# Optimization experiments

Hardware: AMD Instinct MI355X
Metric: run time of the kernel (lower is better)

## Reference

```python
import jax, jax.numpy as jnp
import numpy as np

BLOCK = 32
# MXFP4 grid: exp_bits=2, man_bits=1, exp_bias=1 -> {0, 0.5, 1, 1.5, 2, 3, 4, 6}
GRID = jnp.array([0.0, 0.5, 1.0, 1.5, 2.0, 3.0, 4.0, 6.0], dtype=jnp.float32)
GRID_MAX = 6.0
EPS = 1e-12


def _snap_to_grid(a):
    # nearest-neighbor snap; ties go to the lower grid value (matches torch ref)
    pos = jnp.searchsorted(GRID, a)              # side='left', same as torch default
    lo = jnp.clip(pos - 1, 0, GRID.shape[0] - 1)
    hi = jnp.clip(pos, 0, GRID.shape[0] - 1)
    v_lo = GRID[lo]
    v_hi = GRID[hi]
    return jnp.where(a - v_lo > v_hi - a, v_hi, v_lo)


def quant_act_mxfp4(x):
    orig_shape = x.shape
    xb = x.astype(jnp.float32).reshape(-1, BLOCK)           # [nblk, BLOCK]
    amax = jnp.clip(jnp.max(jnp.abs(xb), axis=-1, keepdims=True), EPS)
    # scale stored in FP16 (quant_act_fp hard-codes scale_dtype='FP16')
    scale = (amax / GRID_MAX).astype(jnp.float16).astype(jnp.float32)
    x_norm = xb / jnp.clip(scale, EPS)
    snapped = _snap_to_grid(jnp.abs(x_norm))
    return (jnp.sign(x_norm) * snapped * scale).reshape(orig_shape)


def setup_inputs() -> dict:
    key = jax.random.key(0)
    k1, k2, k3 = jax.random.split(key, 3)
    x = jax.random.normal(k1, (2, 4096, 4096), dtype=jnp.float32)
    W = jax.random.normal(k2, (11008, 4096), dtype=jnp.float32)
    bias = jax.random.normal(k3, (11008,), dtype=jnp.float32)
    return {"x": x, "W": W, "bias": bias}


def reference(x, W, bias):
    # 1) dynamic per-block MXFP4 activation quantization
    x_q = quant_act_mxfp4(x)                                # [B, S, H]
    # 2) dense GEMM: F.linear(x_q, W, bias)
    return jnp.einsum('bsh,oh->bso', x_q, W) + bias
```

## Files before the change

### kernel.cpp

```cpp
#include <hip/hip_runtime.h>


#define M_DIM 8192
#define K_DIM 4096
#define N_DIM 11008

typedef float floatx4 __attribute__((ext_vector_type(4)));
typedef _Float16 half8 __attribute__((ext_vector_type(8)));


__device__ inline float snap_mxfp4(float a) {
    float lo  = (a <= 0.25f) ? 0.0f : ((a <= 0.75f) ? 0.5f : 1.0f);
    float mid = (a <= 1.75f) ? 1.5f : 2.0f;
    float hi  = (a <= 3.5f)  ? 3.0f : ((a <= 5.0f) ? 4.0f : 6.0f);
    return (a <= 1.25f) ? lo : ((a <= 2.5f) ? mid : hi);
}

__global__ __launch_bounds__(256) void quant_x_kernel(
        const float* __restrict__ x, _Float16* __restrict__ xq) {
    size_t t    = (size_t)blockIdx.x * 256 + threadIdx.x;
    size_t base = t * 8;
    const float4* p = (const float4*)(x + base);
    float4 v0 = p[0];
    float4 v1 = p[1];
    float in[8] = {v0.x, v0.y, v0.z, v0.w, v1.x, v1.y, v1.z, v1.w};

    float a0 = fmaxf(fmaxf(fabsf(in[0]), fabsf(in[1])), fmaxf(fabsf(in[2]), fabsf(in[3])));
    float a1 = fmaxf(fmaxf(fabsf(in[4]), fabsf(in[5])), fmaxf(fabsf(in[6]), fabsf(in[7])));
    float amax = fmaxf(a0, a1);
    amax = fmaxf(amax, __shfl_xor(amax, 1));
    amax = fmaxf(amax, __shfl_xor(amax, 2));
    amax = fmaxf(amax, 1e-12f);

    float scale = (float)(_Float16)(amax / 6.0f);
    float sdiv  = fmaxf(scale, 1e-12f);

    union { _Float16 h[8]; uint4 v; } o;
#pragma unroll
    for (int i = 0; i < 8; ++i) {
        float xn = in[i] / sdiv;
        float s  = snap_mxfp4(fabsf(xn));
        o.h[i]   = (_Float16)copysignf(s * scale, xn);
    }
    *(uint4*)(xq + base) = o.v;
}


__global__ __launch_bounds__(256) void conv_w_kernel(
        const float* __restrict__ W, _Float16* __restrict__ Wq) {
    size_t t    = (size_t)blockIdx.x * 256 + threadIdx.x;
    size_t base = t * 8;
    const float4* p = (const float4*)(W + base);
    float4 v0 = p[0];
    float4 v1 = p[1];
    float in[8] = {v0.x, v0.y, v0.z, v0.w, v1.x, v1.y, v1.z, v1.w};
    union { _Float16 h[8]; uint4 v; } o;
#pragma unroll
    for (int i = 0; i < 8; ++i) o.h[i] = (_Float16)in[i];
    *(uint4*)(Wq + base) = o.v;
}


#define BM 128
#define BN 128
#define BK 32

__global__ __launch_bounds__(256) void gemm_f16_kernel(
        const _Float16* __restrict__ A, const _Float16* __restrict__ B,
        const float* __restrict__ bias, float* __restrict__ C) {
    __shared__ __align__(16) _Float16 sA[BM * BK];
    __shared__ __align__(16) _Float16 sB[BN * BK];

    const int tid   = threadIdx.x;
    const int lane  = tid & 63;
    const int wave  = tid >> 6;
    const int wr    = wave >> 1;
    const int wc    = wave & 1;
    const int mlane = lane & 15;
    const int kq    = lane >> 4;

    const int rowStart = blockIdx.y * BM;
    const int colStart = blockIdx.x * BN;

    const int p0 = tid, p1 = tid + 256;
    const int r0 = p0 >> 2, r1 = p1 >> 2;
    const int kc0 = (p0 & 3) ^ (r0 & 3);
    const int kc1 = (p1 & 3) ^ (r1 & 3);
    const _Float16* aSrc0 = A + (size_t)(rowStart + r0) * K_DIM + kc0 * 8;
    const _Float16* aSrc1 = A + (size_t)(rowStart + r1) * K_DIM + kc1 * 8;
    const _Float16* bSrc0 = B + (size_t)(colStart + r0) * K_DIM + kc0 * 8;
    const _Float16* bSrc1 = B + (size_t)(colStart + r1) * K_DIM + kc1 * 8;

    _Float16* ldsA0 = sA + (wave * 64) * 8;
    _Float16* ldsA1 = sA + (256 + wave * 64) * 8;
    _Float16* ldsB0 = sB + (wave * 64) * 8;
    _Float16* ldsB1 = sB + (256 + wave * 64) * 8;

    int aOff[4], bOff[4];
#pragma unroll
    for (int i = 0; i < 4; ++i) {
        int row = wr * 64 + i * 16 + mlane;
        aOff[i] = (row * 4 + (kq ^ (row & 3))) * 8;
        int col = wc * 64 + i * 16 + mlane;
        bOff[i] = (col * 4 + (kq ^ (col & 3))) * 8;
    }

    floatx4 acc[4][4];
    const floatx4 z4 = {0.f, 0.f, 0.f, 0.f};
#pragma unroll
    for (int i = 0; i < 4; ++i)
#pragma unroll
        for (int j = 0; j < 4; ++j) acc[i][j] = z4;

    for (int k0 = 0; k0 < K_DIM; k0 += BK) {
        __builtin_amdgcn_global_load_lds(
            (const __attribute__((address_space(1))) unsigned int*)(const void*)(aSrc0 + k0),
            (__attribute__((address_space(3))) unsigned int*)(void*)ldsA0, 16, 0, 0);
        __builtin_amdgcn_global_load_lds(
            (const __attribute__((address_space(1))) unsigned int*)(const void*)(aSrc1 + k0),
            (__attribute__((address_space(3))) unsigned int*)(void*)ldsA1, 16, 0, 0);
        __builtin_amdgcn_global_load_lds(
            (const __attribute__((address_space(1))) unsigned int*)(const void*)(bSrc0 + k0),
            (__attribute__((address_space(3))) unsigned int*)(void*)ldsB0, 16, 0, 0);
        __builtin_amdgcn_global_load_lds(
            (const __attribute__((address_space(1))) unsigned int*)(const void*)(bSrc1 + k0),
            (__attribute__((address_space(3))) unsigned int*)(void*)ldsB1, 16, 0, 0);

        __syncthreads();

        half8 af[4], bf[4];
#pragma unroll
        for (int i = 0; i < 4; ++i) {
            af[i] = *(const half8*)(sA + aOff[i]);
            bf[i] = *(const half8*)(sB + bOff[i]);
        }
#pragma unroll
        for (int mt = 0; mt < 4; ++mt)
#pragma unroll
            for (int nt = 0; nt < 4; ++nt)
                acc[mt][nt] = __builtin_amdgcn_mfma_f32_16x16x32_f16(
                    af[mt], bf[nt], acc[mt][nt], 0, 0, 0);

        __syncthreads();
    }

#pragma unroll
    for (int mt = 0; mt < 4; ++mt) {
        int gm = rowStart + wr * 64 + mt * 16 + kq * 4;
#pragma unroll
        for (int nt = 0; nt < 4; ++nt) {
            int gn = colStart + wc * 64 + nt * 16 + mlane;
            float bv = bias[gn];
#pragma unroll
            for (int r = 0; r < 4; ++r)
                C[(size_t)(gm + r) * N_DIM + gn] = acc[mt][nt][r] + bv;
        }
    }
}


extern "C" void kernel_launch(void* const* d_in, const int* in_sizes, int n_in,
                              void* d_out, int out_size, void* d_ws, size_t ws_size,
                              hipStream_t stream) {
    const float* x    = (const float*)d_in[0];
    const float* W    = (const float*)d_in[1];
    const float* bias = (const float*)d_in[2];
    float* out = (float*)d_out;

    _Float16* Aq = (_Float16*)d_ws;
    _Float16* Wq = Aq + (size_t)M_DIM * K_DIM;

    quant_x_kernel<<<16384, 256, 0, stream>>>(x, Aq);
    conv_w_kernel<<<22016, 256, 0, stream>>>(W, Wq);
    gemm_f16_kernel<<<dim3(N_DIM / BN, M_DIM / BM), 256, 0, stream>>>(Aq, Wq, bias, out);
}
```

Measured before the change: 1.475 ms.

## Prefetch next K tile during MFMA, band-swizzle tile order, merge prep kernels

The GEMM main loop now issues the global-to-LDS loads for the next K slice right after the current fragments are read into registers, so the loads overlap the MFMA work instead of waiting behind it. A 1D grid is remapped so N tiles are visited in bands of 32 columns across all M tiles, aiming for better L2 reuse of the weight tiles. The x quantization and W conversion kernels are merged into one launch. The prefetch keeps a single LDS buffer guarded by two barriers, and the remapping adds some index arithmetic per block.

```diff
diff --git a/kernel.cpp b/kernel.cpp
--- a/kernel.cpp
+++ b/kernel.cpp
@@ -16,54 +16,59 @@
     return (a <= 1.25f) ? lo : ((a <= 2.5f) ? mid : hi);
 }
 
-__global__ __launch_bounds__(256) void quant_x_kernel(
-        const float* __restrict__ x, _Float16* __restrict__ xq) {
-    size_t t    = (size_t)blockIdx.x * 256 + threadIdx.x;
-    size_t base = t * 8;
-    const float4* p = (const float4*)(x + base);
-    float4 v0 = p[0];
-    float4 v1 = p[1];
-    float in[8] = {v0.x, v0.y, v0.z, v0.w, v1.x, v1.y, v1.z, v1.w};
-
-    float a0 = fmaxf(fmaxf(fabsf(in[0]), fabsf(in[1])), fmaxf(fabsf(in[2]), fabsf(in[3])));
-    float a1 = fmaxf(fmaxf(fabsf(in[4]), fabsf(in[5])), fmaxf(fabsf(in[6]), fabsf(in[7])));
-    float amax = fmaxf(a0, a1);
-    amax = fmaxf(amax, __shfl_xor(amax, 1));
-    amax = fmaxf(amax, __shfl_xor(amax, 2));
-    amax = fmaxf(amax, 1e-12f);
-
-    float scale = (float)(_Float16)(amax / 6.0f);
-    float sdiv  = fmaxf(scale, 1e-12f);
-
-    union { _Float16 h[8]; uint4 v; } o;
-#pragma unroll
-    for (int i = 0; i < 8; ++i) {
-        float xn = in[i] / sdiv;
-        float s  = snap_mxfp4(fabsf(xn));
-        o.h[i]   = (_Float16)copysignf(s * scale, xn);
-    }
-    *(uint4*)(xq + base) = o.v;
-}
-
-
-__global__ __launch_bounds__(256) void conv_w_kernel(
-        const float* __restrict__ W, _Float16* __restrict__ Wq) {
-    size_t t    = (size_t)blockIdx.x * 256 + threadIdx.x;
-    size_t base = t * 8;
-    const float4* p = (const float4*)(W + base);
-    float4 v0 = p[0];
-    float4 v1 = p[1];
-    float in[8] = {v0.x, v0.y, v0.z, v0.w, v1.x, v1.y, v1.z, v1.w};
-    union { _Float16 h[8]; uint4 v; } o;
-#pragma unroll
-    for (int i = 0; i < 8; ++i) o.h[i] = (_Float16)in[i];
-    *(uint4*)(Wq + base) = o.v;
+#define QUANT_BLOCKS 16384
+#define CONV_BLOCKS  22016
+
+__global__ __launch_bounds__(256) void prep_kernel(
+        const float* __restrict__ x, _Float16* __restrict__ xq,
+        const float* __restrict__ W, _Float16* __restrict__ wq) {
+    if (blockIdx.x < QUANT_BLOCKS) {
+        size_t t    = (size_t)blockIdx.x * 256 + threadIdx.x;
+        size_t base = t * 8;
+        const float4* p = (const float4*)(x + base);
+        float4 v0 = p[0];
+        float4 v1 = p[1];
+        float in[8] = {v0.x, v0.y, v0.z, v0.w, v1.x, v1.y, v1.z, v1.w};
+
+        float a0 = fmaxf(fmaxf(fabsf(in[0]), fabsf(in[1])), fmaxf(fabsf(in[2]), fabsf(in[3])));
+        float a1 = fmaxf(fmaxf(fabsf(in[4]), fabsf(in[5])), fmaxf(fabsf(in[6]), fabsf(in[7])));
+        float amax = fmaxf(a0, a1);
+        amax = fmaxf(amax, __shfl_xor(amax, 1));
+        amax = fmaxf(amax, __shfl_xor(amax, 2));
+        amax = fmaxf(amax, 1e-12f);
+
+        float scale = (float)(_Float16)(amax / 6.0f);
+        float sdiv  = fmaxf(scale, 1e-12f);
+
+        union { _Float16 h[8]; uint4 v; } o;
+#pragma unroll
+        for (int i = 0; i < 8; ++i) {
+            float xn = in[i] / sdiv;
+            float s  = snap_mxfp4(fabsf(xn));
+            o.h[i]   = (_Float16)copysignf(s * scale, xn);
+        }
+        *(uint4*)(xq + base) = o.v;
+    } else {
+        size_t t    = (size_t)(blockIdx.x - QUANT_BLOCKS) * 256 + threadIdx.x;
+        size_t base = t * 8;
+        const float4* p = (const float4*)(W + base);
+        float4 v0 = p[0];
+        float4 v1 = p[1];
+        float in[8] = {v0.x, v0.y, v0.z, v0.w, v1.x, v1.y, v1.z, v1.w};
+        union { _Float16 h[8]; uint4 v; } o;
+#pragma unroll
+        for (int i = 0; i < 8; ++i) o.h[i] = (_Float16)in[i];
+        *(uint4*)(wq + base) = o.v;
+    }
 }
 
 
 #define BM 128
 #define BN 128
 #define BK 32
+#define M_TILES 64
+#define N_TILES 86
+#define BANDW 32
 
 __global__ __launch_bounds__(256) void gemm_f16_kernel(
         const _Float16* __restrict__ A, const _Float16* __restrict__ B,
@@ -79,8 +84,20 @@
     const int mlane = lane & 15;
     const int kq    = lane >> 4;
 
-    const int rowStart = blockIdx.y * BM;
-    const int colStart = blockIdx.x * BN;
+    int pid = blockIdx.x;
+    int mTile, nTile;
+    if (pid < M_TILES * BANDW * 2) {
+        int band = pid >> 11;
+        int rem  = pid & 2047;
+        nTile = (band << 5) + (rem & 31);
+        mTile = rem >> 5;
+    } else {
+        int rem = pid - M_TILES * BANDW * 2;
+        nTile = 64 + rem % 22;
+        mTile = rem / 22;
+    }
+    const int rowStart = mTile * BM;
+    const int colStart = nTile * BN;
 
     const int p0 = tid, p1 = tid + 256;
     const int r0 = p0 >> 2, r1 = p1 >> 2;
@@ -112,20 +129,25 @@
 #pragma unroll
         for (int j = 0; j < 4; ++j) acc[i][j] = z4;
 
+#define ISSUE_LOADS(K0)                                                            \
+    do {                                                                           \
+        __builtin_amdgcn_global_load_lds(                                          \
+            (const __attribute__((address_space(1))) unsigned int*)(const void*)(aSrc0 + (K0)), \
+            (__attribute__((address_space(3))) unsigned int*)(void*)ldsA0, 16, 0, 0); \
+        __builtin_amdgcn_global_load_lds(                                          \
+            (const __attribute__((address_space(1))) unsigned int*)(const void*)(aSrc1 + (K0)), \
+            (__attribute__((address_space(3))) unsigned int*)(void*)ldsA1, 16, 0, 0); \
+        __builtin_amdgcn_global_load_lds(                                          \
+            (const __attribute__((address_space(1))) unsigned int*)(const void*)(bSrc0 + (K0)), \
+            (__attribute__((address_space(3))) unsigned int*)(void*)ldsB0, 16, 0, 0); \
+        __builtin_amdgcn_global_load_lds(                                          \
+            (const __attribute__((address_space(1))) unsigned int*)(const void*)(bSrc1 + (K0)), \
+            (__attribute__((address_space(3))) unsigned int*)(void*)ldsB1, 16, 0, 0); \
+    } while (0)
+
+    ISSUE_LOADS(0);
+
     for (int k0 = 0; k0 < K_DIM; k0 += BK) {
-        __builtin_amdgcn_global_load_lds(
-            (const __attribute__((address_space(1))) unsigned int*)(const void*)(aSrc0 + k0),
-            (__attribute__((address_space(3))) unsigned int*)(void*)ldsA0, 16, 0, 0);
-        __builtin_amdgcn_global_load_lds(
-            (const __attribute__((address_space(1))) unsigned int*)(const void*)(aSrc1 + k0),
-            (__attribute__((address_space(3))) unsigned int*)(void*)ldsA1, 16, 0, 0);
-        __builtin_amdgcn_global_load_lds(
-            (const __attribute__((address_space(1))) unsigned int*)(const void*)(bSrc0 + k0),
-            (__attribute__((address_space(3))) unsigned int*)(void*)ldsB0, 16, 0, 0);
-        __builtin_amdgcn_global_load_lds(
-            (const __attribute__((address_space(1))) unsigned int*)(const void*)(bSrc1 + k0),
-            (__attribute__((address_space(3))) unsigned int*)(void*)ldsB1, 16, 0, 0);
-
         __syncthreads();
 
         half8 af[4], bf[4];
@@ -134,14 +156,17 @@
             af[i] = *(const half8*)(sA + aOff[i]);
             bf[i] = *(const half8*)(sB + bOff[i]);
         }
+
+        __syncthreads();
+
+        if (k0 + BK < K_DIM) ISSUE_LOADS(k0 + BK);
+
 #pragma unroll
         for (int mt = 0; mt < 4; ++mt)
 #pragma unroll
             for (int nt = 0; nt < 4; ++nt)
                 acc[mt][nt] = __builtin_amdgcn_mfma_f32_16x16x32_f16(
                     af[mt], bf[nt], acc[mt][nt], 0, 0, 0);
-
-        __syncthreads();
     }
 
 #pragma unroll
@@ -170,7 +195,6 @@
     _Float16* Aq = (_Float16*)d_ws;
     _Float16* Wq = Aq + (size_t)M_DIM * K_DIM;
 
-    quant_x_kernel<<<16384, 256, 0, stream>>>(x, Aq);
-    conv_w_kernel<<<22016, 256, 0, stream>>>(W, Wq);
-    gemm_f16_kernel<<<dim3(N_DIM / BN, M_DIM / BM), 256, 0, stream>>>(Aq, Wq, bias, out);
-}
+    prep_kernel<<<QUANT_BLOCKS + CONV_BLOCKS, 256, 0, stream>>>(x, Aq, W, Wq);
+    gemm_f16_kernel<<<M_TILES * N_TILES, 256, 0, stream>>>(Aq, Wq, bias, out);
+}
```

After: 1.458 ms. No clear change (-1.2%).
